# Kernel tuning notes

Measured on AMD Instinct MI355X. Metric: run time of the kernel, lower is better.

The kernel has to match this reference:

```python
import jax, jax.numpy as jnp
import numpy as np

D_MODEL = 512
NUM_HEADS = 8
D_K = D_MODEL // NUM_HEADS
LN_EPS = 1e-5


def setup_inputs() -> dict:
    key = jax.random.key(0)
    ks = jax.random.split(key, 11)
    d = D_MODEL
    s = 1.0 / np.sqrt(d)
    return {
        "x": jax.random.normal(ks[0], (4, 2048, d), dtype=jnp.float32),
        "Wq": jax.random.uniform(ks[1], (d, d), jnp.float32, -s, s),
        "bq": jax.random.uniform(ks[2], (d,), jnp.float32, -s, s),
        "Wk": jax.random.uniform(ks[3], (d, d), jnp.float32, -s, s),
        "bk": jax.random.uniform(ks[4], (d,), jnp.float32, -s, s),
        "Wv": jax.random.uniform(ks[5], (d, d), jnp.float32, -s, s),
        "bv": jax.random.uniform(ks[6], (d,), jnp.float32, -s, s),
        "Wo": jax.random.uniform(ks[7], (d, d), jnp.float32, -s, s),
        "bo": jax.random.uniform(ks[8], (d,), jnp.float32, -s, s),
        "gamma": jnp.ones((d,), jnp.float32),
        "beta": jnp.zeros((d,), jnp.float32),
    }


def reference(x, Wq, bq, Wk, bk, Wv, bv, Wo, bo, gamma, beta):
    # x: (B, S, D). Dropout is identity (eval mode).
    B, S, D = x.shape
    H, dk = NUM_HEADS, D_K
    # Linear layers use torch convention: y = x @ W.T + b
    q = (x @ Wq.T + bq).reshape(B, S, H, dk).transpose(0, 2, 1, 3)  # (B,H,S,dk)
    k = (x @ Wk.T + bk).reshape(B, S, H, dk).transpose(0, 2, 1, 3)
    v = (x @ Wv.T + bv).reshape(B, S, H, dk).transpose(0, 2, 1, 3)
    scores = jnp.einsum("bhqd,bhkd->bhqk", q, k) / jnp.sqrt(jnp.float32(dk))
    attn = jax.nn.softmax(scores, axis=-1)
    ctx = jnp.einsum("bhqk,bhkd->bhqd", attn, v)  # (B,H,S,dk)
    ctx = ctx.transpose(0, 2, 1, 3).reshape(B, S, D)
    out = ctx @ Wo.T + bo
    # residual + LayerNorm
    y = x + out
    mu = jnp.mean(y, axis=-1, keepdims=True)
    var = jnp.mean(jnp.square(y - mu), axis=-1, keepdims=True)
    return (y - mu) / jnp.sqrt(var + LN_EPS) * gamma + beta
```

## Files before the change

### kernel.cpp

```cpp
#include <hip/hip_runtime.h>
#include <math.h>

#define D 512
#define NH 8
#define DK 64
#define S 2048
#define BATCH 4
#define N_TOK (BATCH * S)

#define QSCALE 0.18033688f

typedef __bf16 bf16x8 __attribute__((ext_vector_type(8)));
typedef __bf16 bf16x4 __attribute__((ext_vector_type(4)));
typedef float f32x4 __attribute__((ext_vector_type(4)));

#define AS1 __attribute__((address_space(1)))
#define AS3 __attribute__((address_space(3)))

#define OFF_XB   0
#define OFF_WB   8388608
#define OFF_Q    10485760
#define OFF_K    18874368
#define OFF_VT   27262976
#define OFF_CTX  35651584
#define OFF_Y    10485760
#define OFF_FLAG 44040192

static __device__ __forceinline__ bf16x8 ldg8(const __bf16* p) {
    return *(const bf16x8*)p;
}
static __device__ __forceinline__ f32x4 mfma16(bf16x8 a, bf16x8 b, f32x4 c) {
    return __builtin_amdgcn_mfma_f32_16x16x32_bf16(a, b, c, 0, 0, 0);
}
static __device__ __forceinline__ float ldf(const void* p, size_t i, int isf) {
    return isf ? ((const float*)p)[i] : (float)(((const __bf16*)p)[i]);
}
static __device__ __forceinline__ float fexp2(float x) {
#if __has_builtin(__builtin_amdgcn_exp2f)
    return __builtin_amdgcn_exp2f(x);
#else
    return exp2f(x);
#endif
}
static __device__ __forceinline__ unsigned pack_trunc(float e0, float e1) {
    return (__builtin_bit_cast(unsigned, e0) >> 16)
         | (__builtin_bit_cast(unsigned, e1) & 0xFFFF0000u);
}
static __device__ __forceinline__ void gload_lds16(const void* g, void* l) {
    __builtin_amdgcn_global_load_lds((const AS1 char*)g, (AS3 char*)l, 16, 0, 0);
}

__global__ __launch_bounds__(256)
void cvt_kernel(const void* __restrict__ x,  const void* __restrict__ Wq,
                const void* __restrict__ Wk, const void* __restrict__ Wv,
                const void* __restrict__ Wo, __bf16* __restrict__ xb,
                __bf16* __restrict__ Wb, int* __restrict__ flag)
{
    const bf16x8 probe = ldg8((const __bf16*)x + (threadIdx.x & 63) * 8);
    int bad = 0;
#pragma unroll
    for (int j = 0; j < 8; ++j) bad |= !(fabsf((float)probe[j]) <= 64.0f);
    const int isf = __any(bad) ? 1 : 0;
    if (blockIdx.x == 0 && threadIdx.x == 0) *flag = isf;

    const size_t i0 = ((size_t)blockIdx.x * 256 + threadIdx.x) * 8;
    const void* src;
    __bf16* dst;
    size_t off;
    if (i0 < 4194304) {
        src = x; off = i0; dst = xb + i0;
    } else {
        const size_t wrel = i0 - 4194304;
        const size_t w = wrel >> 18;
        src = (w == 0) ? Wq : (w == 1) ? Wk : (w == 2) ? Wv : Wo;
        off = wrel & 262143;
        dst = Wb + wrel;
    }
    bf16x8 r;
    if (isf) {
        const float* f = (const float*)src + off;
#pragma unroll
        for (int j = 0; j < 8; ++j) r[j] = (__bf16)f[j];
    } else {
        r = *(const bf16x8*)((const __bf16*)src + off);
    }
    *(bf16x8*)dst = r;
}

__global__ __launch_bounds__(256)
void qkv_kernel(const __bf16* __restrict__ xb, const __bf16* __restrict__ Wb,
                const void* __restrict__ bq, const void* __restrict__ bk,
                const void* __restrict__ bv, const int* __restrict__ flag,
                __bf16* __restrict__ Q, __bf16* __restrict__ K,
                __bf16* __restrict__ Vt)
{
    __shared__ __align__(16) char smem[24576];

    const int isf = *flag;
    const int tid = threadIdx.x;
    const int w = tid >> 6, l = tid & 63;
    const int lane16 = l & 15, quad = l >> 4;
    const int wm = w >> 1, wn = w & 1;
    const int m0 = blockIdx.x * 128;
    const int by = blockIdx.y;

    const int cwl = w * 64 + l;
    const int g0 = (cwl & 3) ^ ((cwl >> 3) & 3);
    const __bf16* aS0 = xb + (size_t)(m0 + (cwl >> 2)) * D + g0 * 8;
    const __bf16* aS1 = aS0 + (size_t)64 * D;
    const __bf16* bS  = Wb + (size_t)(by * 64 + (cwl >> 2)) * D + g0 * 8;

    const int sw = (quad ^ ((lane16 >> 1) & 3)) * 16;
    const int aoff = (wm * 64 + lane16) * 64 + sw;
    const int boff = 8192 + (wn * 32 + lane16) * 64 + sw;

    f32x4 acc[4][2];
#pragma unroll
    for (int i = 0; i < 4; ++i)
#pragma unroll
        for (int j = 0; j < 2; ++j) acc[i][j] = (f32x4){0,0,0,0};

    gload_lds16(aS0, smem + w * 1024);
    gload_lds16(aS1, smem + 4096 + w * 1024);
    gload_lds16(bS,  smem + 8192 + w * 1024);

    for (int kt = 0; kt < D / 32; ++kt) {
        __syncthreads();

        const char* bufp = smem + (kt & 1) * 12288;
        if (kt + 1 < D / 32) {
            char* nb = smem + ((kt + 1) & 1) * 12288;
            gload_lds16(aS0 + (kt + 1) * 32, nb + w * 1024);
            gload_lds16(aS1 + (kt + 1) * 32, nb + 4096 + w * 1024);
            gload_lds16(bS  + (kt + 1) * 32, nb + 8192 + w * 1024);
        }

        bf16x8 af[4], bf[2];
#pragma unroll
        for (int i = 0; i < 4; ++i) af[i] = *(const bf16x8*)(bufp + aoff + i * 1024);
#pragma unroll
        for (int j = 0; j < 2; ++j) bf[j] = *(const bf16x8*)(bufp + boff + j * 1024);
#pragma unroll
        for (int i = 0; i < 4; ++i)
#pragma unroll
            for (int j = 0; j < 2; ++j)
                acc[i][j] = mfma16(af[i], bf[j], acc[i][j]);
    }

    const int which = by >> 3;
    const int h = by & 7;
    const float qs = (which == 0) ? QSCALE : 1.0f;
    const void* bias = (which == 0) ? bq : (which == 1) ? bk : bv;
    float bvv[2];
#pragma unroll
    for (int j = 0; j < 2; ++j)
        bvv[j] = ldf(bias, h * 64 + wn * 32 + 16 * j + lane16, isf);

    const int bb = m0 >> 11;
    const int ssb = (m0 & (S - 1)) + wm * 64;

    if (which < 2) {
        __bf16* out = ((which == 0) ? Q : K) + ((size_t)(bb * NH + h) * S) * DK;
#pragma unroll
        for (int i = 0; i < 4; ++i)
#pragma unroll
            for (int r = 0; r < 4; ++r) {
                const int ss = ssb + i * 16 + quad * 4 + r;
#pragma unroll
                for (int j = 0; j < 2; ++j)
                    out[(size_t)ss * DK + wn * 32 + 16 * j + lane16] =
                        (__bf16)((acc[i][j][r] + bvv[j]) * qs);
            }
    } else {
#pragma unroll
        for (int i = 0; i < 4; ++i)
#pragma unroll
            for (int j = 0; j < 2; ++j) {
                const int dkc = wn * 32 + 16 * j + lane16;
                __bf16* vp = Vt + ((size_t)(bb * NH + h) * DK + dkc) * S
                                + ssb + i * 16 + quad * 4;
                bf16x4 pkt;
#pragma unroll
                for (int r = 0; r < 4; ++r) pkt[r] = (__bf16)(acc[i][j][r] + bvv[j]);
                *(bf16x4*)vp = pkt;
            }
    }
}

__global__ __launch_bounds__(256)
void attn_kernel(const __bf16* __restrict__ Q, const __bf16* __restrict__ K,
                 const __bf16* __restrict__ Vt, __bf16* __restrict__ ctx)
{
    __shared__ __align__(16) char smem[40960];

    const int tid = threadIdx.x;
    const int w = tid >> 6, l = tid & 63;
    const int lane16 = l & 15, quad = l >> 4;

    const int lin = blockIdx.x;
    const int xcd = lin & 7;
    const int t = lin >> 3;
    const int bh = xcd * 4 + (t >> 5);
    const int qt = t & 31;
    const int b = bh >> 3, h = bh & 7;
    const size_t bhS = (size_t)bh * S;

    const int cwl = w * 64 + l;
    const char* kS[2];
    const char* vS[2];
#pragma unroll
    for (int c = 0; c < 2; ++c) {
        const int s = c * 256 + cwl;
        const int row = s >> 3;
        const int g = (s & 7) ^ (row & 7);
        kS[c] = (const char*)(K + (bhS + row) * DK) + g * 16;
        vS[c] = (const char*)(Vt + ((size_t)bh * DK + row) * S) + g * 16;
    }

    const int qbase = qt * 64 + w * 16;
    const __bf16* Qp = Q + (bhS + qbase + lane16) * DK + quad * 8;
    const bf16x8 qa0 = ldg8(Qp);
    const bf16x8 qa1 = ldg8(Qp + 32);

    bf16x8 aones;
#pragma unroll
    for (int j = 0; j < 8; ++j) aones[j] = (__bf16)1.0f;

    const int x7 = lane16 & 7;
    char* pw = smem + 32768 + w * 2048;
    const int pwoff = lane16 * 128 + ((quad & 1) * 8);
    const int proff = lane16 * 128;

    f32x4 o[4], lacc = (f32x4){0,0,0,0};
#pragma unroll
    for (int tt = 0; tt < 4; ++tt) o[tt] = (f32x4){0,0,0,0};

    gload_lds16(kS[0], smem + w * 1024);
    gload_lds16(kS[1], smem + 4096 + w * 1024);
    gload_lds16(vS[0], smem + 8192 + w * 1024);
    gload_lds16(vS[1], smem + 12288 + w * 1024);

    for (int kc = 0; kc < S / 64; ++kc) {
        __syncthreads();

        const int buf = kc & 1;
        const char* kb = smem + buf * 16384;
        const char* vb = kb + 8192;

        if (kc + 1 < S / 64) {
            char* kb2 = smem + (buf ^ 1) * 16384;
            gload_lds16(kS[0] + (size_t)(kc + 1) * 8192, kb2 + w * 1024);
            gload_lds16(kS[1] + (size_t)(kc + 1) * 8192, kb2 + 4096 + w * 1024);
            gload_lds16(vS[0] + (size_t)(kc + 1) * 128, kb2 + 8192 + w * 1024);
            gload_lds16(vS[1] + (size_t)(kc + 1) * 128, kb2 + 12288 + w * 1024);
        }

#pragma unroll
        for (int tt = 0; tt < 4; ++tt) {
            const int base = (tt * 16 + lane16) * 128;
            const bf16x8 kfA = *(const bf16x8*)(kb + base + ((quad ^ x7) * 16));
            const bf16x8 kfB = *(const bf16x8*)(kb + base + (((quad + 4) ^ x7) * 16));
            f32x4 z = {0,0,0,0};
            z = mfma16(kfA, qa0, z);
            const f32x4 st = mfma16(kfB, qa1, z);
            uint2 pkt;
            pkt.x = pack_trunc(fexp2(st[0]), fexp2(st[1]));
            pkt.y = pack_trunc(fexp2(st[2]), fexp2(st[3]));
            *(uint2*)(pw + pwoff + (((tt * 2 + (quad >> 1)) ^ x7) * 16)) = pkt;
        }

        const bf16x8 bp0 = *(const bf16x8*)(pw + proff + (((0 + quad) ^ x7) * 16));
        const bf16x8 bp1 = *(const bf16x8*)(pw + proff + (((4 + quad) ^ x7) * 16));
        lacc = mfma16(aones, bp0, lacc);
        lacc = mfma16(aones, bp1, lacc);
#pragma unroll
        for (int tt = 0; tt < 4; ++tt) {
            const int base = (tt * 16 + lane16) * 128;
            const bf16x8 vA = *(const bf16x8*)(vb + base + ((quad ^ x7) * 16));
            const bf16x8 vB = *(const bf16x8*)(vb + base + (((quad + 4) ^ x7) * 16));
            o[tt] = mfma16(vA, bp0, o[tt]);
            o[tt] = mfma16(vB, bp1, o[tt]);
        }
    }

    const float inv = 1.0f / lacc[0];
    __bf16* cp = ctx + ((size_t)(b * S + qbase + lane16)) * D + h * DK;
#pragma unroll
    for (int tt = 0; tt < 4; ++tt) {
        bf16x4 pkt;
#pragma unroll
        for (int r = 0; r < 4; ++r) pkt[r] = (__bf16)(o[tt][r] * inv);
        *(bf16x4*)(cp + tt * 16 + quad * 4) = pkt;
    }
}

__global__ __launch_bounds__(256)
void proj_kernel(const __bf16* __restrict__ ctx, const __bf16* __restrict__ Wb,
                 const void* __restrict__ bo, const __bf16* __restrict__ xb,
                 const int* __restrict__ flag, __bf16* __restrict__ y)
{
    __shared__ __align__(16) char smem[16384];

    const int isf = *flag;
    const int tid = threadIdx.x;
    const int w = tid >> 6, l = tid & 63;
    const int lane16 = l & 15, quad = l >> 4;
    const int wm = w >> 1, wn = w & 1;
    const int m0 = blockIdx.x * 64;
    const int n0 = blockIdx.y * 64;

    const __bf16* Wo = Wb + (size_t)3 * 262144;
    const int cwl = w * 64 + l;
    const int g0 = (cwl & 3) ^ ((cwl >> 3) & 3);
    const __bf16* aS = ctx + (size_t)(m0 + (cwl >> 2)) * D + g0 * 8;
    const __bf16* bS = Wo + (size_t)(n0 + (cwl >> 2)) * D + g0 * 8;

    const int sw = (quad ^ ((lane16 >> 1) & 3)) * 16;
    const int aoff = (wm * 32 + lane16) * 64 + sw;
    const int boff = 4096 + (wn * 32 + lane16) * 64 + sw;

    f32x4 acc[2][2];
#pragma unroll
    for (int i = 0; i < 2; ++i)
#pragma unroll
        for (int j = 0; j < 2; ++j) acc[i][j] = (f32x4){0,0,0,0};

    gload_lds16(aS, smem + w * 1024);
    gload_lds16(bS, smem + 4096 + w * 1024);

    for (int kt = 0; kt < D / 32; ++kt) {
        __syncthreads();

        const char* bufp = smem + (kt & 1) * 8192;
        if (kt + 1 < D / 32) {
            char* nb = smem + ((kt + 1) & 1) * 8192;
            gload_lds16(aS + (kt + 1) * 32, nb + w * 1024);
            gload_lds16(bS + (kt + 1) * 32, nb + 4096 + w * 1024);
        }

        bf16x8 af[2], bf[2];
#pragma unroll
        for (int i = 0; i < 2; ++i) af[i] = *(const bf16x8*)(bufp + aoff + i * 1024);
#pragma unroll
        for (int j = 0; j < 2; ++j) bf[j] = *(const bf16x8*)(bufp + boff + j * 1024);
#pragma unroll
        for (int i = 0; i < 2; ++i)
#pragma unroll
            for (int j = 0; j < 2; ++j)
                acc[i][j] = mfma16(af[i], bf[j], acc[i][j]);
    }

    float bvv[2];
#pragma unroll
    for (int j = 0; j < 2; ++j)
        bvv[j] = ldf(bo, n0 + wn * 32 + 16 * j + lane16, isf);

#pragma unroll
    for (int i = 0; i < 2; ++i)
#pragma unroll
        for (int r = 0; r < 4; ++r) {
            const int tok = m0 + wm * 32 + i * 16 + quad * 4 + r;
#pragma unroll
            for (int j = 0; j < 2; ++j) {
                const size_t idx = (size_t)tok * D + n0 + wn * 32 + 16 * j + lane16;
                y[idx] = (__bf16)(acc[i][j][r] + bvv[j] + (float)xb[idx]);
            }
        }
}

__global__ __launch_bounds__(256)
void ln_kernel(const __bf16* __restrict__ y, const void* __restrict__ gamma,
               const void* __restrict__ beta, const int* __restrict__ flag,
               void* __restrict__ out)
{
    const int isf = *flag;
    const int l = threadIdx.x & 63;
    const int tok = blockIdx.x * 4 + (threadIdx.x >> 6);
    const bf16x8 vv = ldg8(y + (size_t)tok * D + l * 8);

    float v[8];
    float sum = 0.f, sq = 0.f;
#pragma unroll
    for (int j = 0; j < 8; ++j) {
        v[j] = (float)vv[j];
        sum += v[j];
        sq  += v[j] * v[j];
    }
#pragma unroll
    for (int msk = 1; msk < 64; msk <<= 1) {
        sum += __shfl_xor(sum, msk);
        sq  += __shfl_xor(sq,  msk);
    }
    const float mean = sum * (1.0f / D);
    const float var  = sq * (1.0f / D) - mean * mean;
    const float rstd = rsqrtf(var + 1e-5f);

    const size_t base = (size_t)tok * D + l * 8;
#pragma unroll
    for (int j = 0; j < 8; ++j) {
        const float g  = ldf(gamma, l * 8 + j, isf);
        const float be = ldf(beta,  l * 8 + j, isf);
        const float r  = ((v[j] - mean) * rstd) * g + be;
        if (isf) ((float*)out)[base + j] = r;
        else     ((__bf16*)out)[base + j] = (__bf16)r;
    }
}

extern "C" void kernel_launch(void* const* d_in, const int* in_sizes, int n_in,
                              void* d_out, int out_size, void* d_ws,
                              size_t ws_size, hipStream_t stream)
{
    const void* x     = d_in[0];
    const void* Wq    = d_in[1];
    const void* bq    = d_in[2];
    const void* Wk    = d_in[3];
    const void* bk    = d_in[4];
    const void* Wv    = d_in[5];
    const void* bv    = d_in[6];
    const void* Wo    = d_in[7];
    const void* bo    = d_in[8];
    const void* gamma = d_in[9];
    const void* beta  = d_in[10];

    char* ws = (char*)d_ws;
    __bf16* xb  = (__bf16*)(ws + OFF_XB);
    __bf16* Wb  = (__bf16*)(ws + OFF_WB);
    __bf16* Qb  = (__bf16*)(ws + OFF_Q);
    __bf16* Kb  = (__bf16*)(ws + OFF_K);
    __bf16* Vtb = (__bf16*)(ws + OFF_VT);
    __bf16* ctx = (__bf16*)(ws + OFF_CTX);
    __bf16* y   = (__bf16*)(ws + OFF_Y);
    int*    flag = (int*)(ws + OFF_FLAG);

    cvt_kernel<<<5242880 / (256 * 8), 256, 0, stream>>>(
        x, Wq, Wk, Wv, Wo, xb, Wb, flag);
    qkv_kernel<<<dim3(N_TOK / 128, 24), 256, 0, stream>>>(
        xb, Wb, bq, bk, bv, flag, Qb, Kb, Vtb);
    attn_kernel<<<dim3(1024), 256, 0, stream>>>(Qb, Kb, Vtb, ctx);
    proj_kernel<<<dim3(N_TOK / 64, D / 64), 256, 0, stream>>>(
        ctx, Wb, bo, xb, flag, y);
    ln_kernel<<<dim3(N_TOK / 4), 256, 0, stream>>>(y, gamma, beta, flag, d_out);
}
```

Before: 192.4 us.

## Fuse fp32-to-bf16 conversion into QKV and output-projection GEMM loads, widen N tiles

Removes the separate conversion kernel: the QKV and output-projection GEMMs now read fp32 (or bf16) inputs directly, convert them in registers and store them to shared memory. The bf16 staging copies of x and the weights disappear. N tiles double (128 columns per block) so the grid shrinks. The cost is register-staged prefetch in place of direct global-to-LDS loads, twice the fp32 global traffic per element, and more accumulators per thread.

After: 215.7 us. +12.1%, slower.

```diff
diff --git a/kernel.cpp b/kernel.cpp
--- a/kernel.cpp
+++ b/kernel.cpp
@@ -17,8 +17,6 @@
 #define AS1 __attribute__((address_space(1)))
 #define AS3 __attribute__((address_space(3)))
 
-#define OFF_XB   0
-#define OFF_WB   8388608
 #define OFF_Q    10485760
 #define OFF_K    18874368
 #define OFF_VT   27262976
@@ -49,134 +47,137 @@
 static __device__ __forceinline__ void gload_lds16(const void* g, void* l) {
     __builtin_amdgcn_global_load_lds((const AS1 char*)g, (AS3 char*)l, 16, 0, 0);
 }
+static __device__ __forceinline__ bf16x8 ld_cvt8(const void* src, size_t eoff,
+                                                 int isf) {
+    if (isf) {
+        const float4 f0 = *(const float4*)((const float*)src + eoff);
+        const float4 f1 = *(const float4*)((const float*)src + eoff + 4);
+        bf16x8 r;
+        r[0] = (__bf16)f0.x; r[1] = (__bf16)f0.y;
+        r[2] = (__bf16)f0.z; r[3] = (__bf16)f0.w;
+        r[4] = (__bf16)f1.x; r[5] = (__bf16)f1.y;
+        r[6] = (__bf16)f1.z; r[7] = (__bf16)f1.w;
+        return r;
+    }
+    return *(const bf16x8*)((const __bf16*)src + eoff);
+}
 
 __global__ __launch_bounds__(256)
-void cvt_kernel(const void* __restrict__ x,  const void* __restrict__ Wq,
-                const void* __restrict__ Wk, const void* __restrict__ Wv,
-                const void* __restrict__ Wo, __bf16* __restrict__ xb,
-                __bf16* __restrict__ Wb, int* __restrict__ flag)
+void qkv_kernel(const void* __restrict__ x,
+                const void* __restrict__ Wq, const void* __restrict__ Wk,
+                const void* __restrict__ Wv,
+                const void* __restrict__ bq, const void* __restrict__ bk,
+                const void* __restrict__ bv,
+                __bf16* __restrict__ Q, __bf16* __restrict__ K,
+                __bf16* __restrict__ Vt, int* __restrict__ flag)
 {
-    const bf16x8 probe = ldg8((const __bf16*)x + (threadIdx.x & 63) * 8);
-    int bad = 0;
-#pragma unroll
-    for (int j = 0; j < 8; ++j) bad |= !(fabsf((float)probe[j]) <= 64.0f);
-    const int isf = __any(bad) ? 1 : 0;
-    if (blockIdx.x == 0 && threadIdx.x == 0) *flag = isf;
-
-    const size_t i0 = ((size_t)blockIdx.x * 256 + threadIdx.x) * 8;
-    const void* src;
-    __bf16* dst;
-    size_t off;
-    if (i0 < 4194304) {
-        src = x; off = i0; dst = xb + i0;
-    } else {
-        const size_t wrel = i0 - 4194304;
-        const size_t w = wrel >> 18;
-        src = (w == 0) ? Wq : (w == 1) ? Wk : (w == 2) ? Wv : Wo;
-        off = wrel & 262143;
-        dst = Wb + wrel;
-    }
-    bf16x8 r;
-    if (isf) {
-        const float* f = (const float*)src + off;
-#pragma unroll
-        for (int j = 0; j < 8; ++j) r[j] = (__bf16)f[j];
-    } else {
-        r = *(const bf16x8*)((const __bf16*)src + off);
-    }
-    *(bf16x8*)dst = r;
-}
-
-__global__ __launch_bounds__(256)
-void qkv_kernel(const __bf16* __restrict__ xb, const __bf16* __restrict__ Wb,
-                const void* __restrict__ bq, const void* __restrict__ bk,
-                const void* __restrict__ bv, const int* __restrict__ flag,
-                __bf16* __restrict__ Q, __bf16* __restrict__ K,
-                __bf16* __restrict__ Vt)
-{
-    __shared__ __align__(16) char smem[24576];
-
-    const int isf = *flag;
+    __shared__ __align__(16) char smem[32768];
+
     const int tid = threadIdx.x;
     const int w = tid >> 6, l = tid & 63;
     const int lane16 = l & 15, quad = l >> 4;
     const int wm = w >> 1, wn = w & 1;
     const int m0 = blockIdx.x * 128;
     const int by = blockIdx.y;
-
-    const int cwl = w * 64 + l;
-    const int g0 = (cwl & 3) ^ ((cwl >> 3) & 3);
-    const __bf16* aS0 = xb + (size_t)(m0 + (cwl >> 2)) * D + g0 * 8;
-    const __bf16* aS1 = aS0 + (size_t)64 * D;
-    const __bf16* bS  = Wb + (size_t)(by * 64 + (cwl >> 2)) * D + g0 * 8;
+    const int which = by >> 3 == 0 ? (by >> 2) : (by >> 2);
+
+    const bf16x8 probe = ldg8((const __bf16*)x + (tid & 63) * 8);
+    int bad = 0;
+#pragma unroll
+    for (int j = 0; j < 8; ++j) bad |= !(fabsf((float)probe[j]) <= 64.0f);
+    const int isf = __any(bad) ? 1 : 0;
+    if (blockIdx.x == 0 && blockIdx.y == 0 && tid == 0) *flag = isf;
+
+    const void* W = (by >> 2) == 0 ? Wq : (by >> 2) == 1 ? Wk : Wv;
+
+    const int srow = tid >> 1, shalf = tid & 1;
+    const int ssw = (srow >> 1) & 3;
+    const int adst  = srow * 64 + (((shalf * 2)     ^ ssw) * 16);
+    const int adst2 = srow * 64 + (((shalf * 2 + 1) ^ ssw) * 16);
+    const size_t aBase = (size_t)(m0 + srow) * D + shalf * 16;
+    const size_t bBase = (size_t)((by & 3) * 128 + srow) * D + shalf * 16;
 
     const int sw = (quad ^ ((lane16 >> 1) & 3)) * 16;
     const int aoff = (wm * 64 + lane16) * 64 + sw;
-    const int boff = 8192 + (wn * 32 + lane16) * 64 + sw;
-
-    f32x4 acc[4][2];
+    const int boff = 8192 + (wn * 64 + lane16) * 64 + sw;
+
+    f32x4 acc[4][4];
 #pragma unroll
     for (int i = 0; i < 4; ++i)
 #pragma unroll
-        for (int j = 0; j < 2; ++j) acc[i][j] = (f32x4){0,0,0,0};
-
-    gload_lds16(aS0, smem + w * 1024);
-    gload_lds16(aS1, smem + 4096 + w * 1024);
-    gload_lds16(bS,  smem + 8192 + w * 1024);
+        for (int j = 0; j < 4; ++j) acc[i][j] = (f32x4){0,0,0,0};
+
+    {
+        *(bf16x8*)(smem + adst)         = ld_cvt8(x, aBase,     isf);
+        *(bf16x8*)(smem + adst2)        = ld_cvt8(x, aBase + 8, isf);
+        *(bf16x8*)(smem + 8192 + adst)  = ld_cvt8(W, bBase,     isf);
+        *(bf16x8*)(smem + 8192 + adst2) = ld_cvt8(W, bBase + 8, isf);
+    }
 
     for (int kt = 0; kt < D / 32; ++kt) {
         __syncthreads();
 
-        const char* bufp = smem + (kt & 1) * 12288;
-        if (kt + 1 < D / 32) {
-            char* nb = smem + ((kt + 1) & 1) * 12288;
-            gload_lds16(aS0 + (kt + 1) * 32, nb + w * 1024);
-            gload_lds16(aS1 + (kt + 1) * 32, nb + 4096 + w * 1024);
-            gload_lds16(bS  + (kt + 1) * 32, nb + 8192 + w * 1024);
-        }
-
-        bf16x8 af[4], bf[2];
+        const char* bufp = smem + (kt & 1) * 16384;
+
+        bf16x8 sA0, sA1, sB0, sB1;
+        const bool pf = (kt + 1 < D / 32);
+        if (pf) {
+            const size_t ka = (size_t)(kt + 1) * 32;
+            sA0 = ld_cvt8(x, aBase + ka,     isf);
+            sA1 = ld_cvt8(x, aBase + ka + 8, isf);
+            sB0 = ld_cvt8(W, bBase + ka,     isf);
+            sB1 = ld_cvt8(W, bBase + ka + 8, isf);
+        }
+
+        bf16x8 af[4], bf[4];
 #pragma unroll
         for (int i = 0; i < 4; ++i) af[i] = *(const bf16x8*)(bufp + aoff + i * 1024);
 #pragma unroll
-        for (int j = 0; j < 2; ++j) bf[j] = *(const bf16x8*)(bufp + boff + j * 1024);
+        for (int j = 0; j < 4; ++j) bf[j] = *(const bf16x8*)(bufp + boff + j * 1024);
 #pragma unroll
         for (int i = 0; i < 4; ++i)
 #pragma unroll
-            for (int j = 0; j < 2; ++j)
+            for (int j = 0; j < 4; ++j)
                 acc[i][j] = mfma16(af[i], bf[j], acc[i][j]);
-    }
-
-    const int which = by >> 3;
-    const int h = by & 7;
-    const float qs = (which == 0) ? QSCALE : 1.0f;
-    const void* bias = (which == 0) ? bq : (which == 1) ? bk : bv;
-    float bvv[2];
-#pragma unroll
-    for (int j = 0; j < 2; ++j)
-        bvv[j] = ldf(bias, h * 64 + wn * 32 + 16 * j + lane16, isf);
+
+        if (pf) {
+            char* nb = smem + ((kt + 1) & 1) * 16384;
+            *(bf16x8*)(nb + adst)         = sA0;
+            *(bf16x8*)(nb + adst2)        = sA1;
+            *(bf16x8*)(nb + 8192 + adst)  = sB0;
+            *(bf16x8*)(nb + 8192 + adst2) = sB1;
+        }
+    }
+
+    const int h = (by * 2 + wn) & 7;
+    const float qs = ((by >> 2) == 0) ? QSCALE : 1.0f;
+    const void* bias = ((by >> 2) == 0) ? bq : ((by >> 2) == 1) ? bk : bv;
+    float bvv[4];
+#pragma unroll
+    for (int j = 0; j < 4; ++j)
+        bvv[j] = ldf(bias, ((by & 3) * 128 + wn * 64 + 16 * j + lane16) & 511, isf);
 
     const int bb = m0 >> 11;
     const int ssb = (m0 & (S - 1)) + wm * 64;
 
-    if (which < 2) {
-        __bf16* out = ((which == 0) ? Q : K) + ((size_t)(bb * NH + h) * S) * DK;
+    if ((by >> 2) < 2) {
+        __bf16* out = (((by >> 2) == 0) ? Q : K) + ((size_t)(bb * NH + h) * S) * DK;
 #pragma unroll
         for (int i = 0; i < 4; ++i)
 #pragma unroll
             for (int r = 0; r < 4; ++r) {
                 const int ss = ssb + i * 16 + quad * 4 + r;
 #pragma unroll
-                for (int j = 0; j < 2; ++j)
-                    out[(size_t)ss * DK + wn * 32 + 16 * j + lane16] =
+                for (int j = 0; j < 4; ++j)
+                    out[(size_t)ss * DK + 16 * j + lane16] =
                         (__bf16)((acc[i][j][r] + bvv[j]) * qs);
             }
     } else {
 #pragma unroll
         for (int i = 0; i < 4; ++i)
 #pragma unroll
-            for (int j = 0; j < 2; ++j) {
-                const int dkc = wn * 32 + 16 * j + lane16;
+            for (int j = 0; j < 4; ++j) {
+                const int dkc = 16 * j + lane16;
                 __bf16* vp = Vt + ((size_t)(bb * NH + h) * DK + dkc) * S
                                 + ssb + i * 16 + quad * 4;
                 bf16x4 pkt;
@@ -295,11 +296,11 @@
 }
 
 __global__ __launch_bounds__(256)
-void proj_kernel(const __bf16* __restrict__ ctx, const __bf16* __restrict__ Wb,
-                 const void* __restrict__ bo, const __bf16* __restrict__ xb,
+void proj_kernel(const __bf16* __restrict__ ctx, const void* __restrict__ Wo,
+                 const void* __restrict__ bo, const void* __restrict__ x,
                  const int* __restrict__ flag, __bf16* __restrict__ y)
 {
-    __shared__ __align__(16) char smem[16384];
+    __shared__ __align__(16) char smem[24576];
 
     const int isf = *flag;
     const int tid = threadIdx.x;
@@ -307,53 +308,69 @@
     const int lane16 = l & 15, quad = l >> 4;
     const int wm = w >> 1, wn = w & 1;
     const int m0 = blockIdx.x * 64;
-    const int n0 = blockIdx.y * 64;
-
-    const __bf16* Wo = Wb + (size_t)3 * 262144;
-    const int cwl = w * 64 + l;
+    const int n0 = blockIdx.y * 128;
+
+    const int cwl = tid;
     const int g0 = (cwl & 3) ^ ((cwl >> 3) & 3);
     const __bf16* aS = ctx + (size_t)(m0 + (cwl >> 2)) * D + g0 * 8;
-    const __bf16* bS = Wo + (size_t)(n0 + (cwl >> 2)) * D + g0 * 8;
+
+    const int srow = tid >> 1, shalf = tid & 1;
+    const int ssw = (srow >> 1) & 3;
+    const int bdst  = 4096 + srow * 64 + (((shalf * 2)     ^ ssw) * 16);
+    const int bdst2 = 4096 + srow * 64 + (((shalf * 2 + 1) ^ ssw) * 16);
+    const size_t bBase = (size_t)(n0 + srow) * D + shalf * 16;
 
     const int sw = (quad ^ ((lane16 >> 1) & 3)) * 16;
     const int aoff = (wm * 32 + lane16) * 64 + sw;
-    const int boff = 4096 + (wn * 32 + lane16) * 64 + sw;
-
-    f32x4 acc[2][2];
+    const int boff = 4096 + (wn * 64 + lane16) * 64 + sw;
+
+    f32x4 acc[2][4];
 #pragma unroll
     for (int i = 0; i < 2; ++i)
 #pragma unroll
-        for (int j = 0; j < 2; ++j) acc[i][j] = (f32x4){0,0,0,0};
+        for (int j = 0; j < 4; ++j) acc[i][j] = (f32x4){0,0,0,0};
 
     gload_lds16(aS, smem + w * 1024);
-    gload_lds16(bS, smem + 4096 + w * 1024);
+    *(bf16x8*)(smem + bdst)  = ld_cvt8(Wo, bBase,     isf);
+    *(bf16x8*)(smem + bdst2) = ld_cvt8(Wo, bBase + 8, isf);
 
     for (int kt = 0; kt < D / 32; ++kt) {
         __syncthreads();
 
-        const char* bufp = smem + (kt & 1) * 8192;
-        if (kt + 1 < D / 32) {
-            char* nb = smem + ((kt + 1) & 1) * 8192;
+        const char* bufp = smem + (kt & 1) * 12288;
+
+        bf16x8 sB0, sB1;
+        const bool pf = (kt + 1 < D / 32);
+        if (pf) {
+            char* nb = smem + ((kt + 1) & 1) * 12288;
             gload_lds16(aS + (kt + 1) * 32, nb + w * 1024);
-            gload_lds16(bS + (kt + 1) * 32, nb + 4096 + w * 1024);
-        }
-
-        bf16x8 af[2], bf[2];
+            const size_t ka = (size_t)(kt + 1) * 32;
+            sB0 = ld_cvt8(Wo, bBase + ka,     isf);
+            sB1 = ld_cvt8(Wo, bBase + ka + 8, isf);
+        }
+
+        bf16x8 af[2], bf[4];
 #pragma unroll
         for (int i = 0; i < 2; ++i) af[i] = *(const bf16x8*)(bufp + aoff + i * 1024);
 #pragma unroll
-        for (int j = 0; j < 2; ++j) bf[j] = *(const bf16x8*)(bufp + boff + j * 1024);
+        for (int j = 0; j < 4; ++j) bf[j] = *(const bf16x8*)(bufp + boff + j * 1024);
 #pragma unroll
         for (int i = 0; i < 2; ++i)
 #pragma unroll
-            for (int j = 0; j < 2; ++j)
+            for (int j = 0; j < 4; ++j)
                 acc[i][j] = mfma16(af[i], bf[j], acc[i][j]);
-    }
-
-    float bvv[2];
-#pragma unroll
-    for (int j = 0; j < 2; ++j)
-        bvv[j] = ldf(bo, n0 + wn * 32 + 16 * j + lane16, isf);
+
+        if (pf) {
+            char* nb = smem + ((kt + 1) & 1) * 12288;
+            *(bf16x8*)(nb + bdst)  = sB0;
+            *(bf16x8*)(nb + bdst2) = sB1;
+        }
+    }
+
+    float bvv[4];
+#pragma unroll
+    for (int j = 0; j < 4; ++j)
+        bvv[j] = ldf(bo, n0 + wn * 64 + 16 * j + lane16, isf);
 
 #pragma unroll
     for (int i = 0; i < 2; ++i)
@@ -361,9 +378,9 @@
         for (int r = 0; r < 4; ++r) {
             const int tok = m0 + wm * 32 + i * 16 + quad * 4 + r;
 #pragma unroll
-            for (int j = 0; j < 2; ++j) {
-                const size_t idx = (size_t)tok * D + n0 + wn * 32 + 16 * j + lane16;
-                y[idx] = (__bf16)(acc[i][j][r] + bvv[j] + (float)xb[idx]);
+            for (int j = 0; j < 4; ++j) {
+                const size_t idx = (size_t)tok * D + n0 + wn * 64 + 16 * j + lane16;
+                y[idx] = (__bf16)(acc[i][j][r] + bvv[j] + ldf(x, idx, isf));
             }
         }
 }
@@ -423,8 +440,6 @@
     const void* beta  = d_in[10];
 
     char* ws = (char*)d_ws;
-    __bf16* xb  = (__bf16*)(ws + OFF_XB);
-    __bf16* Wb  = (__bf16*)(ws + OFF_WB);
     __bf16* Qb  = (__bf16*)(ws + OFF_Q);
     __bf16* Kb  = (__bf16*)(ws + OFF_K);
     __bf16* Vtb = (__bf16*)(ws + OFF_VT);
@@ -432,12 +447,10 @@
     __bf16* y   = (__bf16*)(ws + OFF_Y);
     int*    flag = (int*)(ws + OFF_FLAG);
 
-    cvt_kernel<<<5242880 / (256 * 8), 256, 0, stream>>>(
-        x, Wq, Wk, Wv, Wo, xb, Wb, flag);
-    qkv_kernel<<<dim3(N_TOK / 128, 24), 256, 0, stream>>>(
-        xb, Wb, bq, bk, bv, flag, Qb, Kb, Vtb);
+    qkv_kernel<<<dim3(N_TOK / 128, 12), 256, 0, stream>>>(
+        x, Wq, Wk, Wv, bq, bk, bv, Qb, Kb, Vtb, flag);
     attn_kernel<<<dim3(1024), 256, 0, stream>>>(Qb, Kb, Vtb, ctx);
-    proj_kernel<<<dim3(N_TOK / 64, D / 64), 256, 0, stream>>>(
-        ctx, Wb, bo, xb, flag, y);
+    proj_kernel<<<dim3(N_TOK / 64, 4), 256, 0, stream>>>(
+        ctx, Wo, bo, x, flag, y);
     ln_kernel<<<dim3(N_TOK / 4), 256, 0, stream>>>(y, gamma, beta, flag, d_out);
 }
```
